# Kernel optimization log

Hardware: AMD Instinct MI355X
Metric: run time of the kernel (lower is better)

The kernel has to match this reference:

```python
import jax, jax.numpy as jnp
import numpy as np

MINI_BLOCK = 8
POLY_HALF = np.array([0.02403, -0.2699, 1.17, -2.454, 2.523, -0.08003], dtype=np.float32)


def setup_inputs() -> dict:
    key = jax.random.key(0)
    k1, k2, k3 = jax.random.split(key, 3)
    x = jax.random.uniform(k1, (512, 1024), dtype=jnp.float32)          # [B, in_channel], magnitude in [0,1]
    weight = jax.random.normal(k2, (128, 128, MINI_BLOCK), dtype=jnp.float32)  # [gy, gx, k]
    scale = jax.random.normal(k3, (1, 1, 64, MINI_BLOCK), dtype=jnp.float32)   # [1,1,gx//2,k]
    return {"x": x, "weight": weight, "scale": scale}


def reference(x, weight, scale):
    gy, gx, k = weight.shape
    B = x.shape[0]
    # in_bit=32 / w_bit=32 -> quantizers are identity; in_channel == gx*k -> no zero pad
    xb = x.reshape(B, gx, k)
    xb = xb * xb  # input modulator
    # circulant multiply: torch normalized rfft / unnormalized weight rfft / normalized irfft
    # cancels to plain circular convolution irfft(rfft(w)*rfft(x))
    Xf = jnp.fft.rfft(xb, axis=-1)                # [B, gx, kf] complex
    Wf = jnp.fft.rfft(weight, axis=-1)            # [gy, gx, kf] complex
    xr = jnp.fft.irfft(Wf[None, :, :, :] * Xf[:, None, :, :], n=k, axis=-1)  # [B, gy, gx, k]
    phase = xr
    # polynomial lambda->mag curve (degree 5, highest coeff first), clamped to [0,1]
    c = jnp.asarray(POLY_HALF)
    p = c[0]
    for ci in c[1:]:
        p = p * xr + ci
    xm = jnp.clip(p, 0.0, 1.0)
    # grid_dim_x even -> scale tiled twice along gx
    s = jnp.concatenate([scale, scale], axis=2)   # [1,1,gx,k]
    xm = xm * s
    # photodetection: add_drop=True, balance_weight=False
    out = (2.0 * xm - 1.0).sum(axis=2)            # [B, gy, k]
    out = out.reshape(B, gy * k)                  # out_channel == out_channel_pad, bias=None
    return out, phase
```

## Files before the change

kernel.cpp:

```cpp
#include <hip/hip_runtime.h>


#define NB   512
#define NGY  128
#define NGX  128
#define NK   8

typedef float f32x4 __attribute__((ext_vector_type(4)));

__global__ __launch_bounds__(256, 2) void molg_pipe(
    const float* __restrict__ x,
    const float* __restrict__ w,
    const float* __restrict__ scale,
    float* __restrict__ d_out)
{
    const int lane = threadIdx.x & 63;
    const int wv   = threadIdx.x >> 6;
    const int b    = blockIdx.x >> 3;
    const int gy0  = (blockIdx.x & 7) * 16 + wv * 4;

    const int gxs = lane >> 1;
    const int kq  = lane & 1;

    float* out   = d_out;
    float* phase = d_out + (size_t)NB * NGY * NK;

    const float c0 = 0.02403f, c1 = -0.2699f, c2 = 1.17f,
                c3 = -2.454f,  c4 = 2.523f,  c5 = -0.08003f;

    float y[4][NK];
#pragma unroll
    for (int it = 0; it < 4; ++it) {
        const int gx = 32 * it + gxs;
        const f32x4* xp = reinterpret_cast<const f32x4*>(x + (size_t)b * 1024 + gx * NK);
        f32x4 a = xp[0], c = xp[1];
        float t[NK] = {a[0]*a[0], a[1]*a[1], a[2]*a[2], a[3]*a[3],
                       c[0]*c[0], c[1]*c[1], c[2]*c[2], c[3]*c[3]};
#pragma unroll
        for (int q = 0; q < NK; ++q)
            y[it][q] = kq ? t[(q + 4) & 7] : t[q];
    }

    const f32x4 sve = *reinterpret_cast<const f32x4*>(scale + (size_t)gxs * NK + 4 * kq);
    const f32x4 svo = *reinterpret_cast<const f32x4*>(scale + (size_t)(gxs + 32) * NK + 4 * kq);

    const float* wbase = w + ((size_t)gy0 * NGX + gxs) * NK;
    f32x4 wb[3][2];
#pragma unroll
    for (int s = 0; s < 2; ++s) {
        const f32x4* p = reinterpret_cast<const f32x4*>(
            wbase + (((s >> 2) * NGX + (s & 3) * 32)) * NK);
        wb[s][0] = p[0];
        wb[s][1] = p[1];
    }

    float acc[4][4];
#pragma unroll
    for (int j = 0; j < 4; ++j)
#pragma unroll
        for (int q = 0; q < 4; ++q) acc[j][q] = 0.f;

    f32x4* pbase4 = reinterpret_cast<f32x4*>(
        phase + (((size_t)b * NGY + gy0) * NGX) * NK);

#pragma unroll
    for (int s = 0; s < 16; ++s) {
        if (s < 14) {
            const int t = s + 2;
            const f32x4* p = reinterpret_cast<const f32x4*>(
                wbase + (((t >> 2) * NGX + (t & 3) * 32)) * NK);
            wb[t % 3][0] = p[0];
            wb[t % 3][1] = p[1];
        }
        const int j = s >> 2, it = s & 3;
        const f32x4 wa = wb[s % 3][0], wc = wb[s % 3][1];
        const float wf[NK] = {wa[0], wa[1], wa[2], wa[3], wc[0], wc[1], wc[2], wc[3]};

        float xr[4];
#pragma unroll
        for (int n = 0; n < 4; ++n) {
            float acc_s = 0.f;
#pragma unroll
            for (int m = 0; m < NK; ++m)
                acc_s = fmaf(wf[m], y[it][(n - m) & 7], acc_s);
            xr[n] = acc_s;
        }

        f32x4 q = {xr[0], xr[1], xr[2], xr[3]};
        __builtin_nontemporal_store(q, pbase4 + j * 256 + it * 64 + lane);

        const f32x4 sv = (it & 1) ? svo : sve;
#pragma unroll
        for (int n = 0; n < 4; ++n) {
            float v = xr[n];
            float p = fmaf(c0, v, c1);
            p = fmaf(p, v, c2);
            p = fmaf(p, v, c3);
            p = fmaf(p, v, c4);
            p = fmaf(p, v, c5);
            p = fminf(fmaxf(p, 0.f), 1.f);
            acc[j][n] = fmaf(p, sv[n], acc[j][n]);
        }
    }

#pragma unroll
    for (int off = 2; off < 64; off <<= 1)
#pragma unroll
        for (int j = 0; j < 4; ++j)
#pragma unroll
            for (int n = 0; n < 4; ++n)
                acc[j][n] += __shfl_xor(acc[j][n], off, 64);

#pragma unroll
    for (int j = 0; j < 4; ++j) {
        if (lane < 2) {
            f32x4 v = {fmaf(2.f, acc[j][0], -128.f), fmaf(2.f, acc[j][1], -128.f),
                       fmaf(2.f, acc[j][2], -128.f), fmaf(2.f, acc[j][3], -128.f)};
            *(reinterpret_cast<f32x4*>(out + (size_t)b * 1024 + (gy0 + j) * NK) + lane) = v;
        }
    }
}

extern "C" void kernel_launch(void* const* d_in, const int* in_sizes, int n_in,
                              void* d_out, int out_size, void* d_ws, size_t ws_size,
                              hipStream_t stream) {
    const float* x     = (const float*)d_in[0];
    const float* w     = (const float*)d_in[1];
    const float* scale = (const float*)d_in[2];
    float* out = (float*)d_out;

    dim3 grid(4096);
    dim3 block(256);
    hipLaunchKernelGGL(molg_pipe, grid, block, 0, stream, x, w, scale, out);
}
```

Before: 62.47 us.

## Stage weight tile in LDS and share it across four batch rows per block

Each block now serves four batch rows, one per wave, over a shared slice of four gy rows. That slice's weights are loaded once into shared memory with a barrier, replacing the per-wave register-pipelined global weight prefetch. The goal is to cut redundant global and L2 weight traffic and to raise the occupancy hint from 2 to 4. The cost is 16KB of LDS per block, a __syncthreads, and no overlap between the weight load and compute.

Result: faster. 52.71 us (-15.6%).

```diff
diff --git a/kernel.cpp b/kernel.cpp
--- a/kernel.cpp
+++ b/kernel.cpp
@@ -8,16 +8,21 @@
 
 typedef float f32x4 __attribute__((ext_vector_type(4)));
 
-__global__ __launch_bounds__(256, 2) void molg_pipe(
+__global__ __launch_bounds__(256, 4) void molg_lds(
     const float* __restrict__ x,
     const float* __restrict__ w,
     const float* __restrict__ scale,
     float* __restrict__ d_out)
 {
-    const int lane = threadIdx.x & 63;
-    const int wv   = threadIdx.x >> 6;
-    const int b    = blockIdx.x >> 3;
-    const int gy0  = (blockIdx.x & 7) * 16 + wv * 4;
+    __shared__ f32x4 lw[1024];
+
+    const int tid  = threadIdx.x;
+    const int lane = tid & 63;
+    const int wv   = tid >> 6;
+    const int bg   = blockIdx.x >> 5;
+    const int gs   = blockIdx.x & 31;
+    const int b    = bg * 4 + wv;
+    const int gy0  = gs * 4;
 
     const int gxs = lane >> 1;
     const int kq  = lane & 1;
@@ -27,6 +32,13 @@
 
     const float c0 = 0.02403f, c1 = -0.2699f, c2 = 1.17f,
                 c3 = -2.454f,  c4 = 2.523f,  c5 = -0.08003f;
+
+    {
+        const f32x4* wsrc = reinterpret_cast<const f32x4*>(w + (size_t)gy0 * NGX * NK);
+#pragma unroll
+        for (int u = 0; u < 4; ++u)
+            lw[tid + 256 * u] = wsrc[tid + 256 * u];
+    }
 
     float y[4][NK];
 #pragma unroll
@@ -44,46 +56,33 @@
     const f32x4 sve = *reinterpret_cast<const f32x4*>(scale + (size_t)gxs * NK + 4 * kq);
     const f32x4 svo = *reinterpret_cast<const f32x4*>(scale + (size_t)(gxs + 32) * NK + 4 * kq);
 
-    const float* wbase = w + ((size_t)gy0 * NGX + gxs) * NK;
-    f32x4 wb[3][2];
-#pragma unroll
-    for (int s = 0; s < 2; ++s) {
-        const f32x4* p = reinterpret_cast<const f32x4*>(
-            wbase + (((s >> 2) * NGX + (s & 3) * 32)) * NK);
-        wb[s][0] = p[0];
-        wb[s][1] = p[1];
-    }
-
     float acc[4][4];
 #pragma unroll
     for (int j = 0; j < 4; ++j)
 #pragma unroll
         for (int q = 0; q < 4; ++q) acc[j][q] = 0.f;
 
+    __syncthreads();
+
     f32x4* pbase4 = reinterpret_cast<f32x4*>(
         phase + (((size_t)b * NGY + gy0) * NGX) * NK);
 
 #pragma unroll
     for (int s = 0; s < 16; ++s) {
-        if (s < 14) {
-            const int t = s + 2;
-            const f32x4* p = reinterpret_cast<const f32x4*>(
-                wbase + (((t >> 2) * NGX + (t & 3) * 32)) * NK);
-            wb[t % 3][0] = p[0];
-            wb[t % 3][1] = p[1];
-        }
         const int j = s >> 2, it = s & 3;
-        const f32x4 wa = wb[s % 3][0], wc = wb[s % 3][1];
+
+        const f32x4 wa = lw[j * 256 + it * 64 + gxs * 2];
+        const f32x4 wc = lw[j * 256 + it * 64 + gxs * 2 + 1];
         const float wf[NK] = {wa[0], wa[1], wa[2], wa[3], wc[0], wc[1], wc[2], wc[3]};
 
         float xr[4];
 #pragma unroll
         for (int n = 0; n < 4; ++n) {
-            float acc_s = 0.f;
+            float s_ = 0.f;
 #pragma unroll
             for (int m = 0; m < NK; ++m)
-                acc_s = fmaf(wf[m], y[it][(n - m) & 7], acc_s);
-            xr[n] = acc_s;
+                s_ = fmaf(wf[m], y[it][(n - m) & 7], s_);
+            xr[n] = s_;
         }
 
         f32x4 q = {xr[0], xr[1], xr[2], xr[3]};
@@ -131,5 +130,5 @@
 
     dim3 grid(4096);
     dim3 block(256);
-    hipLaunchKernelGGL(molg_pipe, grid, block, 0, stream, x, w, scale, out);
+    hipLaunchKernelGGL(molg_lds, grid, block, 0, stream, x, w, scale, out);
 }
```
